# Kernel tuning notes

Measured on AMD Instinct MI355X. Metric: run time of the kernel, lower is better.

## Reference

```python
import jax, jax.numpy as jnp
import numpy as np

EPS = 1e-6
N_HEAD = 16

def alibi_slopes(n_head):
    # standard ALiBi geometric slopes for power-of-2 head counts
    start = 2.0 ** (-8.0 / n_head)
    return (start ** np.arange(1, n_head + 1)).astype(np.float32)

def rsig(x):
    # rational sigmoid sigma(x) = 0.5 * (x / (|x| + 1) + 1)
    return 0.5 * (x / (jnp.abs(x) + 1.0) + 1.0)

def mr_norm(x, w):
    # RationalMR: x / (mean(|x|) + eps) * weight
    return x / (jnp.mean(jnp.abs(x), axis=-1, keepdims=True) + EPS) * w


def setup_inputs() -> dict:
    key = jax.random.key(0)
    ks = jax.random.split(key, 6)
    d_model, d_ffn = 1024, 4096
    B, T = 1, 2048
    x = jax.random.normal(ks[0], (B, T, d_model), dtype=jnp.float32)
    s = 0.02
    w_qkv = jax.random.normal(ks[1], (3 * d_model, d_model), dtype=jnp.float32) * s
    w_out = jax.random.normal(ks[2], (d_model, d_model), dtype=jnp.float32) * s
    w_merged = jax.random.normal(ks[3], (2 * d_ffn, d_model), dtype=jnp.float32) * s
    w3 = jax.random.normal(ks[4], (d_model, d_ffn), dtype=jnp.float32) * s
    norm1_w = jnp.ones((d_model,), dtype=jnp.float32)
    norm2_w = jnp.ones((d_model,), dtype=jnp.float32)
    return {"x": x, "w_qkv": w_qkv, "w_out": w_out, "w_merged": w_merged,
            "w3": w3, "norm1_w": norm1_w, "norm2_w": norm2_w}


def reference(x, w_qkv, w_out, w_merged, w3, norm1_w, norm2_w):
    B, T, C = x.shape
    H = N_HEAD
    D = C // H
    scale = 1.0 / jnp.sqrt(jnp.float32(D))

    # --- attention sub-block ---
    h = mr_norm(x, norm1_w)
    qkv = (h @ w_qkv.T).reshape(B, T, 3, H, D).transpose(2, 0, 3, 1, 4)  # [3,B,H,T,D]
    q, k, v = qkv[0], qkv[1], qkv[2]
    scores = jnp.einsum('bhtd,bhsd->bhts', q, k) * scale  # [B,H,T,T]
    pos = jnp.arange(T)
    rel = jnp.abs(pos[:, None] - pos[None, :]).astype(jnp.float32)
    slopes = jnp.asarray(alibi_slopes(H))
    scores = scores - rel[None, None] * slopes[None, :, None, None]
    causal = pos[None, :] > pos[:, None]  # mask j > i
    scores = jnp.where(causal[None, None], jnp.float32(-10000.0), scores)
    # rational softmax: sigma(s)^4 / (sum sigma(s)^4 + eps)
    p4 = rsig(scores) ** 4
    probs = p4 / (jnp.sum(p4, axis=-1, keepdims=True) + EPS)
    attn = jnp.einsum('bhts,bhsd->bhtd', probs, v)  # [B,H,T,D]
    attn = attn.transpose(0, 2, 1, 3).reshape(B, T, C)
    x = x + attn @ w_out.T

    # --- FFN sub-block (rational SwiGLU) ---
    h2 = mr_norm(x, norm2_w)
    merged = h2 @ w_merged.T
    gate, val = jnp.split(merged, 2, axis=-1)
    hidden = gate * rsig(gate) * val
    x = x + hidden @ w3.T
    return x
```

## Files before the change

### kernel.cpp

```cpp
#include <hip/hip_runtime.h>
#include <hip/hip_bf16.h>
#include <stdint.h>

typedef unsigned int u32;
typedef unsigned short u16;
typedef __attribute__((ext_vector_type(8))) short bf16x8;
typedef __attribute__((ext_vector_type(4))) float f32x4;

#define MFMA(a, b, c) __builtin_amdgcn_mfma_f32_16x16x32_bf16(a, b, c, 0, 0, 0)

__device__ __forceinline__ u16 f2bf(float f) {
  u32 u = __float_as_uint(f);
  return (u16)((u + 0x7FFFu + ((u >> 16) & 1u)) >> 16);
}
__device__ __forceinline__ float bf2f(u16 h) {
  return __uint_as_float(((u32)h) << 16);
}
__device__ __forceinline__ float rsig_fast(float sc) {
  return 0.5f + 0.5f * sc * __builtin_amdgcn_rcpf(fabsf(sc) + 1.f);
}
__device__ __forceinline__ void async16(void* lds, const void* g) {
  __builtin_amdgcn_global_load_lds((const __attribute__((address_space(1))) u32*)g,
                                   (__attribute__((address_space(3))) u32*)lds, 16, 0, 0);
}

__global__ __launch_bounds__(256) void to_bf16(const float* __restrict__ src,
                                               u16* __restrict__ dst) {
  const size_t i = (size_t)blockIdx.x * 256 + threadIdx.x;
  const float4 a = ((const float4*)src)[2 * i];
  const float4 b = ((const float4*)src)[2 * i + 1];
  ushort4 o0, o1;
  o0.x = f2bf(a.x); o0.y = f2bf(a.y); o0.z = f2bf(a.z); o0.w = f2bf(a.w);
  o1.x = f2bf(b.x); o1.y = f2bf(b.y); o1.z = f2bf(b.z); o1.w = f2bf(b.w);
  ((ushort4*)dst)[2 * i] = o0;
  ((ushort4*)dst)[2 * i + 1] = o1;
}

__global__ __launch_bounds__(256) void mrnorm(const float* __restrict__ x,
                                              const float* __restrict__ wg,
                                              u16* __restrict__ out) {
  const int row = blockIdx.x;
  const int tid = threadIdx.x;
  const float4 v = ((const float4*)(x + (size_t)row * 1024))[tid];
  float s = fabsf(v.x) + fabsf(v.y) + fabsf(v.z) + fabsf(v.w);
#pragma unroll
  for (int off = 1; off < 64; off <<= 1) s += __shfl_xor(s, off);
  __shared__ float red[4];
  if ((tid & 63) == 0) red[tid >> 6] = s;
  __syncthreads();
  const float inv = 1.f / ((red[0] + red[1] + red[2] + red[3]) * (1.f / 1024.f) + 1e-6f);
  const float4 g = ((const float4*)wg)[tid];
  ushort4 o;
  o.x = f2bf(v.x * inv * g.x);
  o.y = f2bf(v.y * inv * g.y);
  o.z = f2bf(v.z * inv * g.z);
  o.w = f2bf(v.w * inv * g.w);
  ((ushort4*)out)[(size_t)row * 256 + tid] = o;
}

template <int EPI, bool DBUF>
__global__ __launch_bounds__(256) void gemm_bt(const u16* __restrict__ A, int lda,
                                               const u16* __restrict__ B, int ldb,
                                               void* __restrict__ C,
                                               const float* __restrict__ resid,
                                               int M, int N, int K) {
  __shared__ __align__(16) u16 As[(DBUF ? 2 : 1) * 128 * 64];
  __shared__ __align__(16) u16 Bs[(DBUF ? 2 : 1) * 128 * 64];
  const int tid = threadIdx.x;
  const int lane = tid & 63;
  const int w = tid >> 6;
  const int wr = (w >> 1) << 6;
  const int wc = (w & 1) << 6;
  const int nbn = N >> 7;
  const int m0 = (blockIdx.x / nbn) << 7;
  const int n0 = (blockIdx.x % nbn) << 7;
  const int l15 = lane & 15;
  const int lhi = lane >> 4;
  A += (size_t)blockIdx.y * K;
  B += (size_t)blockIdx.y * K;

  f32x4 acc[4][4] = {};

  auto stage = [&](int buf, int k0) {
#pragma unroll
    for (int p = 0; p < 4; ++p) {
      const int c = p * 256 + tid;
      const int row = c >> 3;
      const int cb = (c & 7) << 4;
      const int src = cb ^ ((row & 7) << 4);
      async16((char*)As + buf * 16384 + c * 16,
              (const char*)A + ((size_t)(m0 + row) * lda + k0) * 2 + src);
      async16((char*)Bs + buf * 16384 + c * 16,
              (const char*)B + ((size_t)(n0 + row) * ldb + k0) * 2 + src);
    }
  };
  auto compute = [&](int buf) {
#pragma unroll
    for (int kk = 0; kk < 2; ++kk) {
      bf16x8 af[4], bfr[4];
#pragma unroll
      for (int m = 0; m < 4; ++m) {
        const int row = wr + (m << 4) + l15;
        const int off = row * 128 + (((kk << 6) + (lhi << 4)) ^ ((row & 7) << 4));
        af[m] = *(const bf16x8*)((const char*)As + buf * 16384 + off);
      }
#pragma unroll
      for (int n = 0; n < 4; ++n) {
        const int row = wc + (n << 4) + l15;
        const int off = row * 128 + (((kk << 6) + (lhi << 4)) ^ ((row & 7) << 4));
        bfr[n] = *(const bf16x8*)((const char*)Bs + buf * 16384 + off);
      }
#pragma unroll
      for (int m = 0; m < 4; ++m)
#pragma unroll
        for (int n = 0; n < 4; ++n)
          acc[m][n] = MFMA(af[m], bfr[n], acc[m][n]);
    }
  };

  if (DBUF) {
    stage(0, 0);
    __syncthreads();
    int cur = 0;
    for (int k0 = 0; k0 < K; k0 += 64) {
      if (k0 + 64 < K) stage(cur ^ 1, k0 + 64);
      compute(cur);
      __syncthreads();
      cur ^= 1;
    }
  } else {
    for (int k0 = 0; k0 < K; k0 += 64) {
      stage(0, k0);
      __syncthreads();
      compute(0);
      __syncthreads();
    }
  }

  u16* Cp = (u16*)C + (size_t)blockIdx.y * M * N;
#pragma unroll
  for (int m = 0; m < 4; ++m) {
#pragma unroll
    for (int n = 0; n < 4; ++n) {
      const int col = n0 + wc + (n << 4) + l15;
#pragma unroll
      for (int r = 0; r < 4; ++r) {
        const int row = m0 + wr + (m << 4) + (lhi << 2) + r;
        const float v = acc[m][n][r];
        if (EPI == 0) {
          Cp[(size_t)row * N + col] = f2bf(v);
        } else {
          const size_t idx = (size_t)row * N + col;
          ((float*)C)[idx] = resid[idx] + v;
        }
      }
    }
  }
}

__global__ __launch_bounds__(256) void gemm_ffn1(const u16* __restrict__ A,
                                                 const u16* __restrict__ B,
                                                 u16* __restrict__ hid) {
  __shared__ __align__(16) u16 As[128 * 64];
  __shared__ __align__(16) u16 Bg[128 * 64];
  __shared__ __align__(16) u16 Bv[128 * 64];
  const int tid = threadIdx.x;
  const int lane = tid & 63;
  const int w = tid >> 6;
  const int wr = (w >> 1) << 6;
  const int wc = (w & 1) << 6;
  const int m0 = (blockIdx.x >> 5) << 7;
  const int n0 = (blockIdx.x & 31) << 7;
  const int l15 = lane & 15;
  const int lhi = lane >> 4;

  f32x4 ag[4][4] = {};
  f32x4 av[4][4] = {};

  for (int k0 = 0; k0 < 1024; k0 += 64) {
#pragma unroll
    for (int p = 0; p < 4; ++p) {
      const int c = p * 256 + tid;
      const int row = c >> 3;
      const int cb = (c & 7) << 4;
      const int src = cb ^ ((row & 7) << 4);
      async16((char*)As + c * 16, (const char*)A + ((size_t)(m0 + row) * 1024 + k0) * 2 + src);
      async16((char*)Bg + c * 16, (const char*)B + ((size_t)(n0 + row) * 1024 + k0) * 2 + src);
      async16((char*)Bv + c * 16, (const char*)B + ((size_t)(4096 + n0 + row) * 1024 + k0) * 2 + src);
    }
    __syncthreads();
#pragma unroll
    for (int kk = 0; kk < 2; ++kk) {
      bf16x8 af[4], bg[4], bv[4];
#pragma unroll
      for (int m = 0; m < 4; ++m) {
        const int row = wr + (m << 4) + l15;
        const int off = row * 128 + (((kk << 6) + (lhi << 4)) ^ ((row & 7) << 4));
        af[m] = *(const bf16x8*)((const char*)As + off);
      }
#pragma unroll
      for (int n = 0; n < 4; ++n) {
        const int row = wc + (n << 4) + l15;
        const int off = row * 128 + (((kk << 6) + (lhi << 4)) ^ ((row & 7) << 4));
        bg[n] = *(const bf16x8*)((const char*)Bg + off);
        bv[n] = *(const bf16x8*)((const char*)Bv + off);
      }
#pragma unroll
      for (int m = 0; m < 4; ++m)
#pragma unroll
        for (int n = 0; n < 4; ++n) {
          ag[m][n] = MFMA(af[m], bg[n], ag[m][n]);
          av[m][n] = MFMA(af[m], bv[n], av[m][n]);
        }
    }
    __syncthreads();
  }

#pragma unroll
  for (int m = 0; m < 4; ++m) {
#pragma unroll
    for (int n = 0; n < 4; ++n) {
      const int col = n0 + wc + (n << 4) + l15;
#pragma unroll
      for (int r = 0; r < 4; ++r) {
        const int row = m0 + wr + (m << 4) + (lhi << 2) + r;
        const float g = ag[m][n][r];
        const float v = av[m][n][r];
        hid[(size_t)row * 4096 + col] = f2bf(g * rsig_fast(g) * v);
      }
    }
  }
}

__global__ __launch_bounds__(256) void splitk_reduce(const u16* __restrict__ part,
                                                     const float* __restrict__ resid,
                                                     float* __restrict__ out) {
  const size_t i = ((size_t)blockIdx.x * 256 + threadIdx.x) * 8;
  const float4 r0 = *(const float4*)(resid + i);
  const float4 r1 = *(const float4*)(resid + i + 4);
  float acc[8] = {r0.x, r0.y, r0.z, r0.w, r1.x, r1.y, r1.z, r1.w};
#pragma unroll
  for (int c = 0; c < 4; ++c) {
    const uint4 p = *(const uint4*)(part + (size_t)c * 2097152 + i);
    const u16* ps = (const u16*)&p;
#pragma unroll
    for (int j = 0; j < 8; ++j) acc[j] += bf2f(ps[j]);
  }
  float4 o0 = {acc[0], acc[1], acc[2], acc[3]};
  float4 o1 = {acc[4], acc[5], acc[6], acc[7]};
  *(float4*)(out + i) = o0;
  *(float4*)(out + i + 4) = o1;
}

__global__ __launch_bounds__(256) void transpose_v(const u16* __restrict__ qkv,
                                                   u16* __restrict__ vt) {
  __shared__ __align__(16) u16 tile[64][72];
  const int head = blockIdx.x >> 5;
  const int t0 = (blockIdx.x & 31) << 6;
  const int tid = threadIdx.x;
  const int row = tid >> 2;
  const int cb = (tid & 3) << 4;
  const u16* src = qkv + (size_t)(t0 + row) * 3072 + 2048 + head * 64 + cb;
  *(uint4*)&tile[row][cb] = *(const uint4*)src;
  *(uint4*)&tile[row][cb + 8] = *(const uint4*)(src + 8);
  __syncthreads();
  u16 buf[16];
#pragma unroll
  for (int j = 0; j < 16; ++j) buf[j] = tile[cb + j][row];
  u16* dst = vt + (size_t)(head * 64 + row) * 2048 + t0 + cb;
  *(uint4*)dst = *(const uint4*)&buf[0];
  *(uint4*)(dst + 8) = *(const uint4*)&buf[8];
}

__global__ __launch_bounds__(256) void attn_part(const u16* __restrict__ qkv,
                                                 const u16* __restrict__ vt,
                                                 u16* __restrict__ pnum,
                                                 float* __restrict__ pden) {
  const int id = blockIdx.x;
  const int head = id & 15;
  const int rem = id >> 4;
  int a, g;
  if (rem < 32)      { a = 3; g = rem; }
  else if (rem < 56) { a = 2; g = rem - 32; }
  else if (rem < 72) { a = 1; g = rem - 56; }
  else               { a = 0; g = rem - 72; }
  const int qb = (a << 3) + g / (a + 1);
  const int c = g - (g / (a + 1)) * (a + 1);
  const int slot = head * 80 + ((a * (a + 1)) << 2) + (qb - (a << 3)) * (a + 1) + c;

  __shared__ __align__(16) u16 Ks[2][64 * 64];
  __shared__ __align__(16) u16 Vs[2][64 * 64];
  __shared__ __align__(16) u16 QP[4][16 * 64];
  const int tid = threadIdx.x;
  const int lane = tid & 63;
  const int w = tid >> 6;
  const int l15 = lane & 15;
  const int lhi = lane >> 4;
  const int qbase = qb << 6;
  const float slope = exp2f(-0.5f * (float)(head + 1));

  auto stageKV = [&](int buf, int s0) {
#pragma unroll
    for (int p = 0; p < 2; ++p) {
      const int cc = p * 256 + tid;
      const int row = cc >> 3;
      const int cb = (cc & 7) << 4;
      const int src = cb ^ ((row & 7) << 4);
      async16((char*)Ks[buf] + cc * 16,
              (const char*)qkv + ((size_t)(s0 + row) * 3072 + 1024 + head * 64) * 2 + src);
      async16((char*)Vs[buf] + cc * 16,
              (const char*)vt + ((size_t)(head * 64 + row) * 2048 + s0) * 2 + src);
    }
  };

  const int sfirst = c << 9;
  const int smax = min(qbase, sfirst + 448);
#pragma unroll
  for (int p = 0; p < 2; ++p) {
    const int cc = p * 256 + tid;
    const int row = cc >> 3;
    const int cb = (cc & 7) << 4;
    const int src = cb ^ ((row & 7) << 4);
    async16((char*)QP + cc * 16,
            (const char*)qkv + ((size_t)(qbase + row) * 3072 + head * 64) * 2 + src);
  }
  stageKV(0, sfirst);
  __syncthreads();

  bf16x8 qf[2];
#pragma unroll
  for (int kk = 0; kk < 2; ++kk) {
    const int row = (w << 4) + l15;
    const int off = row * 128 + (((kk << 6) + (lhi << 4)) ^ ((row & 7) << 4));
    qf[kk] = *(const bf16x8*)((const char*)QP + off);
  }

  f32x4 oacc[4] = {};
  float rs[4] = {0.f, 0.f, 0.f, 0.f};
  u16* pw = (u16*)QP[w];
  int cur = 0;

  for (int s0 = sfirst; s0 <= smax; s0 += 64) {
    if (s0 + 64 <= smax) stageKV(cur ^ 1, s0 + 64);
    const char* Kc = (const char*)Ks[cur];
    const char* Vc = (const char*)Vs[cur];

    bf16x8 kf[4][2];
#pragma unroll
    for (int bb = 0; bb < 4; ++bb)
#pragma unroll
      for (int kk = 0; kk < 2; ++kk) {
        const int row = (bb << 4) + l15;
        const int off = row * 128 + (((kk << 6) + (lhi << 4)) ^ ((row & 7) << 4));
        kf[bb][kk] = *(const bf16x8*)(Kc + off);
      }
    f32x4 sa[4];
#pragma unroll
    for (int bb = 0; bb < 4; ++bb) {
      f32x4 z = {0.f, 0.f, 0.f, 0.f};
      z = MFMA(qf[0], kf[bb][0], z);
      sa[bb] = MFMA(qf[1], kf[bb][1], z);
    }
#pragma unroll
    for (int bb = 0; bb < 4; ++bb) {
      const int s_abs = s0 + (bb << 4) + l15;
#pragma unroll
      for (int r = 0; r < 4; ++r) {
        const int prow = (lhi << 2) + r;
        const int q_abs = qbase + (w << 4) + prow;
        float p4 = 0.f;
        if (s_abs <= q_abs) {
          const float sc = sa[bb][r] * 0.125f - slope * (float)(q_abs - s_abs);
          const float t = rsig_fast(sc);
          const float t2 = t * t;
          p4 = t2 * t2;
        }
        rs[r] += p4;
        const int pcol2 = ((bb << 4) + l15) << 1;
        const int poff = prow * 128 + (pcol2 ^ ((prow & 7) << 4));
        *(u16*)((char*)pw + poff) = f2bf(p4);
      }
    }
    bf16x8 pf[2];
#pragma unroll
    for (int kk = 0; kk < 2; ++kk) {
      const int row = l15;
      const int off = row * 128 + (((kk << 6) + (lhi << 4)) ^ ((row & 7) << 4));
      pf[kk] = *(const bf16x8*)((const char*)pw + off);
    }
#pragma unroll
    for (int db = 0; db < 4; ++db) {
#pragma unroll
      for (int kk = 0; kk < 2; ++kk) {
        const int row = (db << 4) + l15;
        const int off = row * 128 + (((kk << 6) + (lhi << 4)) ^ ((row & 7) << 4));
        const bf16x8 vf = *(const bf16x8*)(Vc + off);
        oacc[db] = MFMA(pf[kk], vf, oacc[db]);
      }
    }
    __syncthreads();
    cur ^= 1;
  }

#pragma unroll
  for (int r = 0; r < 4; ++r) {
    float v = rs[r];
    v += __shfl_xor(v, 1);
    v += __shfl_xor(v, 2);
    v += __shfl_xor(v, 4);
    v += __shfl_xor(v, 8);
    rs[r] = v;
  }
  if (l15 == 0) {
#pragma unroll
    for (int r = 0; r < 4; ++r)
      pden[(size_t)slot * 64 + (w << 4) + (lhi << 2) + r] = rs[r];
  }
  __syncthreads();
#pragma unroll
  for (int db = 0; db < 4; ++db)
#pragma unroll
    for (int r = 0; r < 4; ++r)
      pw[((lhi << 2) + r) * 64 + (db << 4) + l15] = f2bf(oacc[db][r]);
  __syncthreads();
  {
    const int row = lane >> 2;
    const int cb = (lane & 3) << 4;
    const u16* s = pw + row * 64 + cb;
    const uint4 d0 = *(const uint4*)s;
    const uint4 d1 = *(const uint4*)(s + 8);
    u16* dst = pnum + (size_t)slot * 4096 + ((w << 4) + row) * 64 + cb;
    *(uint4*)dst = d0;
    *(uint4*)(dst + 8) = d1;
  }
}

__global__ __launch_bounds__(256) void attn_merge(const u16* __restrict__ pnum,
                                                  const float* __restrict__ pden,
                                                  u16* __restrict__ out) {
  const int head = blockIdx.x >> 5;
  const int qb = blockIdx.x & 31;
  const int nc = (qb >> 3) + 1;
  const int a = qb >> 3, b = qb & 7;
  const int slot0 = head * 80 + ((a * (a + 1)) << 2) + b * (a + 1);
  const int tid = threadIdx.x;
  const int row = tid >> 2;
  const int c0 = (tid & 3) << 4;

  float acc[16] = {};
  float den = 0.f;
  for (int ci = 0; ci < nc; ++ci) {
    const int slot = slot0 + ci;
    den += pden[(size_t)slot * 64 + row];
    const u16* np = pnum + (size_t)slot * 4096 + row * 64 + c0;
    const uint4 n0 = *(const uint4*)np;
    const uint4 n1 = *(const uint4*)(np + 8);
    const u16* ns0 = (const u16*)&n0;
    const u16* ns1 = (const u16*)&n1;
#pragma unroll
    for (int j = 0; j < 8; ++j) {
      acc[j] += bf2f(ns0[j]);
      acc[8 + j] += bf2f(ns1[j]);
    }
  }
  const float inv = 1.f / (den + 1e-6f);
  u16 ob[16];
#pragma unroll
  for (int j = 0; j < 16; ++j) ob[j] = f2bf(acc[j] * inv);
  u16* dst = out + (size_t)((qb << 6) + row) * 1024 + head * 64 + c0;
  *(uint4*)dst = *(const uint4*)&ob[0];
  *(uint4*)(dst + 8) = *(const uint4*)&ob[8];
}

extern "C" void kernel_launch(void* const* d_in, const int* in_sizes, int n_in,
                              void* d_out, int out_size, void* d_ws, size_t ws_size,
                              hipStream_t stream) {
  const float* x     = (const float*)d_in[0];
  const float* wqkv  = (const float*)d_in[1];
  const float* wout  = (const float*)d_in[2];
  const float* wmer  = (const float*)d_in[3];
  const float* w3    = (const float*)d_in[4];
  const float* n1w   = (const float*)d_in[5];
  const float* n2w   = (const float*)d_in[6];
  char* ws = (char*)d_ws;

  u16*   WQKV = (u16*)(ws + 0);
  u16*   WOUT = (u16*)(ws + 6291456);
  u16*   WMER = (u16*)(ws + 8388608);
  u16*   W3B  = (u16*)(ws + 25165824);
  float* X1   = (float*)(ws + 33554432);
  u16*   QKV  = (u16*)(ws + 41943040);
  u16*   VT   = (u16*)(ws + 54525952);
  u16*   ATTN = (u16*)(ws + 58720256);
  u16*   PNUM = (u16*)(ws + 62914560);
  float* PDEN = (float*)(ws + 73400320);
  u16*   HID  = (u16*)(ws + 41943040);
  u16*   PART = (u16*)(ws + 8388608);
  u16*   H    = (u16*)(ws + 75497472);
  u16*   H2   = (u16*)(ws + 75497472);

  to_bf16<<<1536, 256, 0, stream>>>(wqkv, WQKV);
  to_bf16<<<512, 256, 0, stream>>>(wout, WOUT);
  to_bf16<<<4096, 256, 0, stream>>>(wmer, WMER);
  to_bf16<<<2048, 256, 0, stream>>>(w3, W3B);

  mrnorm<<<2048, 256, 0, stream>>>(x, n1w, H);
  gemm_bt<0, true><<<16 * 24, 256, 0, stream>>>(H, 1024, WQKV, 1024, QKV, nullptr,
                                                2048, 3072, 1024);
  transpose_v<<<512, 256, 0, stream>>>(QKV, VT);
  attn_part<<<1280, 256, 0, stream>>>(QKV, VT, PNUM, PDEN);
  attn_merge<<<512, 256, 0, stream>>>(PNUM, PDEN, ATTN);
  gemm_bt<1, true><<<16 * 8, 256, 0, stream>>>(ATTN, 1024, WOUT, 1024, X1, x,
                                               2048, 1024, 1024);

  mrnorm<<<2048, 256, 0, stream>>>(X1, n2w, H2);
  gemm_ffn1<<<512, 256, 0, stream>>>(H2, WMER, HID);
  gemm_bt<0, true><<<dim3(16 * 8, 4), 256, 0, stream>>>(HID, 4096, W3B, 4096, PART,
                                                        nullptr, 2048, 1024, 1024);
  splitk_reduce<<<1024, 256, 0, stream>>>(PART, X1, (float*)d_out);
}
```

Before: 200.9 us.

## Double-buffer FFN1 gate/value GEMM and halve N tile to 64

The fused gate/value FFN1 GEMM now double-buffers its LDS tiles, issuing async global-to-LDS loads for the next K slice while computing on the current one. It also shrinks the N tile from 128 to 64 columns and doubles the grid to 1024 blocks. This keeps LDS at 64KB, lowers accumulator registers, and gives more blocks to spread across CUs. The trade-off is lower arithmetic intensity per block, since A tiles are reloaded twice as often.

```diff
diff --git a/kernel.cpp b/kernel.cpp
--- a/kernel.cpp
+++ b/kernel.cpp
@@ -161,65 +161,85 @@
 __global__ __launch_bounds__(256) void gemm_ffn1(const u16* __restrict__ A,
                                                  const u16* __restrict__ B,
                                                  u16* __restrict__ hid) {
-  __shared__ __align__(16) u16 As[128 * 64];
-  __shared__ __align__(16) u16 Bg[128 * 64];
-  __shared__ __align__(16) u16 Bv[128 * 64];
+  __shared__ __align__(16) u16 As[2][128 * 64];
+  __shared__ __align__(16) u16 Bg[2][64 * 64];
+  __shared__ __align__(16) u16 Bv[2][64 * 64];
   const int tid = threadIdx.x;
   const int lane = tid & 63;
   const int w = tid >> 6;
   const int wr = (w >> 1) << 6;
-  const int wc = (w & 1) << 6;
-  const int m0 = (blockIdx.x >> 5) << 7;
-  const int n0 = (blockIdx.x & 31) << 7;
+  const int wc = (w & 1) << 5;
+  const int m0 = (blockIdx.x >> 6) << 7;
+  const int n0 = (blockIdx.x & 63) << 6;
   const int l15 = lane & 15;
   const int lhi = lane >> 4;
 
-  f32x4 ag[4][4] = {};
-  f32x4 av[4][4] = {};
-
-  for (int k0 = 0; k0 < 1024; k0 += 64) {
+  f32x4 ag[4][2] = {};
+  f32x4 av[4][2] = {};
+
+  auto stage = [&](int buf, int k0) {
 #pragma unroll
     for (int p = 0; p < 4; ++p) {
       const int c = p * 256 + tid;
       const int row = c >> 3;
       const int cb = (c & 7) << 4;
       const int src = cb ^ ((row & 7) << 4);
-      async16((char*)As + c * 16, (const char*)A + ((size_t)(m0 + row) * 1024 + k0) * 2 + src);
-      async16((char*)Bg + c * 16, (const char*)B + ((size_t)(n0 + row) * 1024 + k0) * 2 + src);
-      async16((char*)Bv + c * 16, (const char*)B + ((size_t)(4096 + n0 + row) * 1024 + k0) * 2 + src);
-    }
-    __syncthreads();
+      async16((char*)As[buf] + c * 16,
+              (const char*)A + ((size_t)(m0 + row) * 1024 + k0) * 2 + src);
+    }
+#pragma unroll
+    for (int p = 0; p < 2; ++p) {
+      const int c = p * 256 + tid;
+      const int row = c >> 3;
+      const int cb = (c & 7) << 4;
+      const int src = cb ^ ((row & 7) << 4);
+      async16((char*)Bg[buf] + c * 16,
+              (const char*)B + ((size_t)(n0 + row) * 1024 + k0) * 2 + src);
+      async16((char*)Bv[buf] + c * 16,
+              (const char*)B + ((size_t)(4096 + n0 + row) * 1024 + k0) * 2 + src);
+    }
+  };
+  auto compute = [&](int buf) {
 #pragma unroll
     for (int kk = 0; kk < 2; ++kk) {
-      bf16x8 af[4], bg[4], bv[4];
+      bf16x8 af[4], bgf[2], bvf[2];
 #pragma unroll
       for (int m = 0; m < 4; ++m) {
         const int row = wr + (m << 4) + l15;
         const int off = row * 128 + (((kk << 6) + (lhi << 4)) ^ ((row & 7) << 4));
-        af[m] = *(const bf16x8*)((const char*)As + off);
-      }
-#pragma unroll
-      for (int n = 0; n < 4; ++n) {
+        af[m] = *(const bf16x8*)((const char*)As[buf] + off);
+      }
+#pragma unroll
+      for (int n = 0; n < 2; ++n) {
         const int row = wc + (n << 4) + l15;
         const int off = row * 128 + (((kk << 6) + (lhi << 4)) ^ ((row & 7) << 4));
-        bg[n] = *(const bf16x8*)((const char*)Bg + off);
-        bv[n] = *(const bf16x8*)((const char*)Bv + off);
+        bgf[n] = *(const bf16x8*)((const char*)Bg[buf] + off);
+        bvf[n] = *(const bf16x8*)((const char*)Bv[buf] + off);
       }
 #pragma unroll
       for (int m = 0; m < 4; ++m)
 #pragma unroll
-        for (int n = 0; n < 4; ++n) {
-          ag[m][n] = MFMA(af[m], bg[n], ag[m][n]);
-          av[m][n] = MFMA(af[m], bv[n], av[m][n]);
+        for (int n = 0; n < 2; ++n) {
+          ag[m][n] = MFMA(af[m], bgf[n], ag[m][n]);
+          av[m][n] = MFMA(af[m], bvf[n], av[m][n]);
         }
     }
+  };
+
+  stage(0, 0);
+  __syncthreads();
+  int cur = 0;
+  for (int k0 = 0; k0 < 1024; k0 += 64) {
+    if (k0 + 64 < 1024) stage(cur ^ 1, k0 + 64);
+    compute(cur);
     __syncthreads();
+    cur ^= 1;
   }
 
 #pragma unroll
   for (int m = 0; m < 4; ++m) {
 #pragma unroll
-    for (int n = 0; n < 4; ++n) {
+    for (int n = 0; n < 2; ++n) {
       const int col = n0 + wc + (n << 4) + l15;
 #pragma unroll
       for (int r = 0; r < 4; ++r) {
@@ -514,7 +534,7 @@
                                                2048, 1024, 1024);
 
   mrnorm<<<2048, 256, 0, stream>>>(X1, n2w, H2);
-  gemm_ffn1<<<512, 256, 0, stream>>>(H2, WMER, HID);
+  gemm_ffn1<<<1024, 256, 0, stream>>>(H2, WMER, HID);
   gemm_bt<0, true><<<dim3(16 * 8, 4), 256, 0, stream>>>(HID, 4096, W3B, 4096, PART,
                                                         nullptr, 2048, 1024, 1024);
   splitk_reduce<<<1024, 256, 0, stream>>>(PART, X1, (float*)d_out);
```

Result: faster. 180.3 us (-10.3%).
